# Kernel optimization log

Measured on AMD Instinct MI355X. Metric: run time of the kernel, lower is better.

## Reference

```python
import jax, jax.numpy as jnp
import numpy as np

L, N, K = 12, 4096, 8   # tree levels, padded nodes per level, max children
V, E, H = 50000, 300, 300


def setup_inputs() -> dict:
    key = jax.random.key(0)
    ks = jax.random.split(key, 24)
    word_ids = jax.random.randint(ks[0], (L, N), 0, V)
    child_idx = jax.random.randint(ks[1], (L, N, K), 0, N)
    child_mask = (jax.random.uniform(ks[2], (L, N, K)) < 0.7).astype(jnp.float32)
    child_mask = child_mask.at[0].set(0.0)  # level 0 nodes are leaves (no children)
    s_e = 1.0 / np.sqrt(E)
    s_h = 1.0 / np.sqrt(H)
    inp = {
        'word_ids': word_ids,
        'child_idx': child_idx,
        'child_mask': child_mask,
        'embedding': jax.random.normal(ks[3], (V, E), jnp.float32),
    }
    for t, g in enumerate(['i', 'f', 'o', 'u']):
        inp['w_' + g] = jax.random.normal(ks[4 + 4 * t], (H, E), jnp.float32) * s_e
        inp['b_w' + g] = jax.random.normal(ks[5 + 4 * t], (H,), jnp.float32) * s_e
        inp['u_' + g] = jax.random.normal(ks[6 + 4 * t], (H, H), jnp.float32) * s_h
        inp['b_u' + g] = jax.random.normal(ks[7 + 4 * t], (H,), jnp.float32) * s_h
    return inp


def _lin(x, W, b):
    # torch nn.Linear: x @ W.T + b
    return jnp.matmul(x, W.T) + b


def reference(word_ids, child_idx, child_mask, embedding,
              w_i, b_wi, u_i, b_ui, w_f, b_wf, u_f, b_uf,
              w_o, b_wo, u_o, b_uo, w_u, b_wu, u_u, b_uu):
    n = word_ids.shape[1]
    h_dim = w_i.shape[0]
    dt = embedding.dtype

    def step(carry, level):
        h_prev, c_prev = carry           # [N, H] from previous tree level
        wids, cidx, cmask = level        # [N], [N, K], [N, K]
        x = embedding[wids]              # [N, E]
        h_k = h_prev[cidx]               # [N, K, H] variable-arity child gather
        c_k = c_prev[cidx]               # [N, K, H]
        m = cmask[..., None]             # [N, K, 1]
        # per-child forget gate: sigmoid(w_f(x_j) + u_f(h_k))
        f = jax.nn.sigmoid(_lin(x, w_f, b_wf)[:, None, :] + _lin(h_k, u_f, b_uf))
        h_tilde = jnp.sum(m * h_k, axis=1)        # child-sum of hidden states
        sum_c = jnp.sum(m * f * c_k, axis=1)      # gated child cell sum
        i = jax.nn.sigmoid(_lin(x, w_i, b_wi) + _lin(h_tilde, u_i, b_ui))
        o = jax.nn.sigmoid(_lin(x, w_o, b_wo) + _lin(h_tilde, u_o, b_uo))
        u = jnp.tanh(_lin(x, w_u, b_wu) + _lin(h_tilde, u_u, b_uu))
        c = i * u + sum_c
        h = o * jnp.tanh(c)
        return (h, c), None

    init = (jnp.zeros((n, h_dim), dt), jnp.zeros((n, h_dim), dt))
    (h, c), _ = jax.lax.scan(step, init, (word_ids, child_idx, child_mask))
    return h, c
```

## Files before the change

### kernel.cpp

```cpp
#include <hip/hip_runtime.h>
#include <cmath>
#include <cstdint>


#define NN    4096
#define HH    300
#define KK    8
#define LVLS  12
#define KP    320
#define MTOT  49152
#define NW    1280

typedef __bf16  bf16x8 __attribute__((ext_vector_type(8)));
typedef float   f32x4  __attribute__((ext_vector_type(4)));

#define GAS __attribute__((address_space(1)))
#define LAS __attribute__((address_space(3)))

__device__ __forceinline__ float sigmoidf_(float x) {
    return 1.0f / (1.0f + expf(-x));
}
__device__ __forceinline__ ushort f2bf(float f) {
    union { float f; uint32_t u; } v; v.f = f;
    return (ushort)((v.u + 0x7fffu + ((v.u >> 16) & 1u)) >> 16);
}
__device__ __forceinline__ float bf2f(ushort u) {
    union { uint32_t u; float f; } v; v.u = ((uint32_t)u) << 16;
    return v.f;
}

__global__ __launch_bounds__(256)
void pack_and_stage(
    const float* __restrict__ wi, const float* __restrict__ bwi,
    const float* __restrict__ ui, const float* __restrict__ bui,
    const float* __restrict__ wf, const float* __restrict__ bwf,
    const float* __restrict__ uf, const float* __restrict__ buf_,
    const float* __restrict__ wo, const float* __restrict__ bwo,
    const float* __restrict__ uo, const float* __restrict__ buo,
    const float* __restrict__ wu, const float* __restrict__ bwu,
    const float* __restrict__ uu, const float* __restrict__ buu,
    ushort* __restrict__ W4, ushort* __restrict__ Ufp, ushort* __restrict__ WzU,
    float* __restrict__ BZ, float* __restrict__ Bwf, float* __restrict__ BUF,
    ushort* __restrict__ Hk,
    const int* __restrict__ word_ids, const float* __restrict__ emb,
    ushort* __restrict__ X)
{
    const int b = blockIdx.x;
    if (b >= 3527) {
        int idx = (b - 3527) * 256 + threadIdx.x;
        int kb = idx / MTOT, row = idx % MTOT;
        const int k0 = kb * 8;
        ushort o[8];
        if (kb < 37) {
            const float4* p = reinterpret_cast<const float4*>(
                emb + (size_t)word_ids[row] * 300 + k0);
            float4 v0 = p[0], v1 = p[1];
            o[0] = f2bf(v0.x); o[1] = f2bf(v0.y); o[2] = f2bf(v0.z); o[3] = f2bf(v0.w);
            o[4] = f2bf(v1.x); o[5] = f2bf(v1.y); o[6] = f2bf(v1.z); o[7] = f2bf(v1.w);
        } else if (kb == 37) {
            const float4 v0 = *reinterpret_cast<const float4*>(
                emb + (size_t)word_ids[row] * 300 + k0);
            o[0] = f2bf(v0.x); o[1] = f2bf(v0.y); o[2] = f2bf(v0.z); o[3] = f2bf(v0.w);
            o[4] = o[5] = o[6] = o[7] = 0;
        } else {
            o[0] = o[1] = o[2] = o[3] = o[4] = o[5] = o[6] = o[7] = 0;
        }
        ushort* dst = X + ((size_t)kb * MTOT + row) * 8;
        ushort4 a; a.x = o[0]; a.y = o[1]; a.z = o[2]; a.w = o[3];
        ushort4 c; c.x = o[4]; c.y = o[5]; c.z = o[6]; c.w = o[7];
        *reinterpret_cast<ushort4*>(dst)     = a;
        *reinterpret_cast<ushort4*>(dst + 4) = c;
        return;
    }
    int t = b * 256 + threadIdx.x;
    if (t < 409600) {
        int gate = t / 102400, rem = t % 102400;
        int r = rem / 320, k = rem % 320;
        const float* W = (gate == 0) ? wf : (gate == 1) ? wi
                       : (gate == 2) ? wo : wu;
        float v = (r < 300 && k < 300) ? W[r * 300 + k] : 0.f;
        W4[((size_t)(k >> 3) * NW + gate * 320 + r) * 8 + (k & 7)] = f2bf(v);
    } else if (t < 512000) {
        int x = t - 409600, r = x / 320, k = x % 320;
        Ufp[((size_t)(k >> 3) * KP + r) * 8 + (k & 7)] =
            f2bf((r < 300 && k < 300) ? uf[r * 300 + k] : 0.f);
    } else if (t < 819200) {
        int x = t - 512000;
        int g = x / 102400, rem = x % 102400;
        int r = rem / 320, k = rem % 320;
        const float* U = (g == 0) ? ui : (g == 1) ? uo : uu;
        WzU[(((size_t)g * 40 + (k >> 3)) * KP + r) * 8 + (k & 7)] =
            f2bf((r < 300 && k < 300) ? U[r * 300 + k] : 0.f);
    } else if (t < 820160) {
        int x = t - 819200, g = x / KP, r = x % KP;
        const float* bw = (g == 0) ? bwi : (g == 1) ? bwo : bwu;
        const float* bu = (g == 0) ? bui : (g == 1) ? buo : buu;
        BZ[x] = (r < 300) ? bw[r] + bu[r] : 0.f;
    } else if (t < 820480) {
        int r = t - 820160;
        Bwf[r] = (r < 300) ? bwf[r] : 0.f;
    } else if (t < 820800) {
        int r = t - 820480;
        BUF[r] = (r < 300) ? buf_[r] : 0.f;
    } else if (t < 902720) {
        int x = t - 820800;
        int row = x / 20, pe = x % 20;
        int k = 300 + pe;
        Hk[((size_t)(k >> 3) * NN + row) * 8 + (k & 7)] = 0;
    }
}

__global__ __launch_bounds__(256)
void zx_all_kernel(const ushort* __restrict__ Xp, const ushort* __restrict__ W4,
                   const float* __restrict__ Bwf, ushort* __restrict__ ZW)
{
    __shared__ __attribute__((aligned(16))) ushort As[2][4][128][8];
    __shared__ __attribute__((aligned(16))) ushort Bs[2][4][128][8];

    const int b  = blockIdx.x;
    const int bj = (b % 8) * 480 + b / 8;
    const int m0 = (bj / 10) * 128, n0 = (bj % 10) * 128;

    const int t = threadIdx.x, l = t & 63, w = t >> 6;
    const int m_off = (w >> 1) * 64, n_off = (w & 1) * 64;
    const int kq = l >> 4, lr = l & 15;

    f32x4 acc[4][4] = {};

    auto STAGE = [&](int buf, int s) {
        #pragma unroll
        for (int c = 0; c < 2; ++c) {
            const int slot = t + 256 * c;
            const int kb = slot >> 7, row = slot & 127;
            const ushort* src = Xp + ((size_t)(s * 4 + kb) * MTOT + m0 + row) * 8;
            __builtin_amdgcn_global_load_lds((const GAS void*)src,
                (LAS void*)&As[buf][kb][row][0], 16, 0, 0);
        }
        #pragma unroll
        for (int c = 0; c < 2; ++c) {
            const int slot = t + 256 * c;
            const int kb = slot >> 7, row = slot & 127;
            const ushort* src = W4 + ((size_t)(s * 4 + kb) * NW + n0 + row) * 8;
            __builtin_amdgcn_global_load_lds((const GAS void*)src,
                (LAS void*)&Bs[buf][kb][row][0], 16, 0, 0);
        }
    };
    auto COMPUTE = [&](int buf) {
        bf16x8 af[4], bfr[4];
        #pragma unroll
        for (int mi = 0; mi < 4; ++mi)
            af[mi] = *reinterpret_cast<const bf16x8*>(
                &As[buf][kq][m_off + mi * 16 + lr][0]);
        #pragma unroll
        for (int ni = 0; ni < 4; ++ni)
            bfr[ni] = *reinterpret_cast<const bf16x8*>(
                &Bs[buf][kq][n_off + ni * 16 + lr][0]);
        #pragma unroll
        for (int mi = 0; mi < 4; ++mi)
            #pragma unroll
            for (int ni = 0; ni < 4; ++ni)
                acc[mi][ni] = __builtin_amdgcn_mfma_f32_16x16x32_bf16(
                    af[mi], bfr[ni], acc[mi][ni], 0, 0, 0);
    };

    STAGE(0, 0);
    #pragma unroll
    for (int s = 0; s < 9; ++s) {
        STAGE((s + 1) & 1, s + 1);
        asm volatile("s_waitcnt vmcnt(4)" ::: "memory");
        __builtin_amdgcn_s_barrier();
        COMPUTE(s & 1);
        __builtin_amdgcn_s_barrier();
    }
    asm volatile("s_waitcnt vmcnt(0)" ::: "memory");
    __builtin_amdgcn_s_barrier();
    COMPUTE(1);

    const int col = l & 15, r0 = (l >> 4) * 4;
    #pragma unroll
    for (int mi = 0; mi < 4; ++mi) {
        #pragma unroll
        for (int ni = 0; ni < 4; ++ni) {
            const int gn = n0 + n_off + ni * 16 + col;
            const float bb = (gn < 320) ? Bwf[gn] : 0.f;
            #pragma unroll
            for (int r = 0; r < 4; ++r) {
                const int gm = m0 + m_off + mi * 16 + r0 + r;
                ZW[(size_t)gm * NW + gn] = f2bf(acc[mi][ni][r] + bb);
            }
        }
    }
}

__global__ __launch_bounds__(256)
void fp_kernel(const ushort* __restrict__ Hk, const ushort* __restrict__ Ufp,
               const float* __restrict__ BUFb, ushort* __restrict__ FP)
{
    __shared__ __attribute__((aligned(16))) ushort As[2][8][64][8];
    __shared__ __attribute__((aligned(16))) ushort Bs[2][8][32][8];

    const int b  = blockIdx.x;
    const int bj = (b % 8) * 80 + b / 8;
    const int m0 = (bj / 10) * 64, j0 = (bj % 10) * 32;

    const int t = threadIdx.x, w = t >> 6, l = t & 63;
    const int kq = l >> 4, lr = l & 15;
    const int m_off = (w >> 1) * 32, j_off = (w & 1) * 16;

    f32x4 acc[2] = {};

    auto STAGE = [&](int buf, int s) {
        #pragma unroll
        for (int c = 0; c < 2; ++c) {
            const int slot = t + 256 * c;
            const int kb = slot >> 6, row = slot & 63;
            const ushort* src = Hk + ((size_t)(s * 8 + kb) * NN + m0 + row) * 8;
            __builtin_amdgcn_global_load_lds((const GAS void*)src,
                (LAS void*)&As[buf][kb][row][0], 16, 0, 0);
        }
        {
            const int kb = t >> 5, row = t & 31;
            const ushort* src = Ufp + ((size_t)(s * 8 + kb) * KP + j0 + row) * 8;
            __builtin_amdgcn_global_load_lds((const GAS void*)src,
                (LAS void*)&Bs[buf][kb][row][0], 16, 0, 0);
        }
    };
    auto COMPUTE = [&](int buf) {
        #pragma unroll
        for (int kk = 0; kk < 2; ++kk) {
            const int kc = kk * 4 + kq;
            bf16x8 af[2], bf;
            #pragma unroll
            for (int mi = 0; mi < 2; ++mi)
                af[mi] = *reinterpret_cast<const bf16x8*>(
                    &As[buf][kc][m_off + mi * 16 + lr][0]);
            bf = *reinterpret_cast<const bf16x8*>(
                    &Bs[buf][kc][j_off + lr][0]);
            #pragma unroll
            for (int mi = 0; mi < 2; ++mi)
                acc[mi] = __builtin_amdgcn_mfma_f32_16x16x32_bf16(
                    af[mi], bf, acc[mi], 0, 0, 0);
        }
    };

    STAGE(0, 0);
    #pragma unroll
    for (int s = 0; s < 4; ++s) {
        STAGE((s + 1) & 1, s + 1);
        asm volatile("s_waitcnt vmcnt(3)" ::: "memory");
        __builtin_amdgcn_s_barrier();
        COMPUTE(s & 1);
        __builtin_amdgcn_s_barrier();
    }
    asm volatile("s_waitcnt vmcnt(0)" ::: "memory");
    __builtin_amdgcn_s_barrier();
    COMPUTE(0);

    const int col = l & 15, r0 = (l >> 4) * 4;
    const int gn = j0 + j_off + col;
    if (gn < 300) {
        const float bb = BUFb[gn];
        #pragma unroll
        for (int mi = 0; mi < 2; ++mi)
            #pragma unroll
            for (int r = 0; r < 4; ++r)
                FP[(size_t)(m0 + m_off + mi * 16 + r0 + r) * KP + gn] =
                    f2bf(acc[mi][r] + bb);
    }
}

__global__ __launch_bounds__(320)
void reduce_kernel(const ushort* __restrict__ Hbf, const float* __restrict__ Cst,
                   const ushort* __restrict__ FP, const ushort* __restrict__ ZWlev,
                   const int* __restrict__ cidx, const float* __restrict__ cmask,
                   ushort* __restrict__ HTp, float* __restrict__ SC)
{
    const int x = threadIdx.x;
    const int ty = threadIdx.y;
    const int n = blockIdx.x * 4 + ty;
    __shared__ int   ch[4][KK];
    __shared__ float mk[4][KK];
    if (x < KK) {
        ch[ty][x] = cidx[n * KK + x];
        mk[ty][x] = cmask[n * KK + x];
    }
    __syncthreads();
    if (x >= 75) {
        ushort4 z; z.x = z.y = z.z = z.w = 0;
        const int pi = x - 75;
        const int kb = 37 + ((pi + 1) >> 1);
        const int off = ((pi & 1) ^ 1) * 4;
        *reinterpret_cast<ushort4*>(
            HTp + ((size_t)kb * NN + n) * 8 + off) = z;
        return;
    }
    const int h = x * 4;

    ushort4 hu[KK]; ushort4 fu[KK]; float4 cv[KK];
    #pragma unroll
    for (int k = 0; k < KK; ++k) {
        const size_t cr = (size_t)ch[ty][k];
        hu[k] = *reinterpret_cast<const ushort4*>(&Hbf[cr * KP + h]);
        fu[k] = *reinterpret_cast<const ushort4*>(&FP [cr * KP + h]);
        cv[k] = *reinterpret_cast<const float4*>(&Cst[cr * HH + h]);
    }

    ushort4 wxu = *reinterpret_cast<const ushort4*>(&ZWlev[(size_t)n * NW + h]);
    const float wx0 = bf2f(wxu.x), wx1 = bf2f(wxu.y),
                wx2 = bf2f(wxu.z), wx3 = bf2f(wxu.w);
    float ht0 = 0.f, ht1 = 0.f, ht2 = 0.f, ht3 = 0.f;
    float sc0 = 0.f, sc1 = 0.f, sc2 = 0.f, sc3 = 0.f;

    #pragma unroll
    for (int k = 0; k < KK; ++k) {
        const float m = mk[ty][k];
        if (m != 0.f) {
            ht0 += m * bf2f(hu[k].x); ht1 += m * bf2f(hu[k].y);
            ht2 += m * bf2f(hu[k].z); ht3 += m * bf2f(hu[k].w);
            sc0 += m * sigmoidf_(wx0 + bf2f(fu[k].x)) * cv[k].x;
            sc1 += m * sigmoidf_(wx1 + bf2f(fu[k].y)) * cv[k].y;
            sc2 += m * sigmoidf_(wx2 + bf2f(fu[k].z)) * cv[k].z;
            sc3 += m * sigmoidf_(wx3 + bf2f(fu[k].w)) * cv[k].w;
        }
    }
    ushort4 ho; ho.x = f2bf(ht0); ho.y = f2bf(ht1); ho.z = f2bf(ht2); ho.w = f2bf(ht3);
    *reinterpret_cast<ushort4*>(
        HTp + ((size_t)(x >> 1) * NN + n) * 8 + (x & 1) * 4) = ho;
    float4 so; so.x = sc0; so.y = sc1; so.z = sc2; so.w = sc3;
    *reinterpret_cast<float4*>(&SC[(size_t)n * KP + h]) = so;
}

__global__ __launch_bounds__(256)
void zgemm(const ushort* __restrict__ HTp, const ushort* __restrict__ WzU,
           const float* __restrict__ BZ, const float* __restrict__ SC,
           const ushort* __restrict__ ZXlev,
           float* __restrict__ cdst, ushort* __restrict__ Hb,
           ushort* __restrict__ Hk, float* __restrict__ hdst)
{
    __shared__ __attribute__((aligned(16))) ushort As[2][8][64][8];
    __shared__ __attribute__((aligned(16))) ushort Bs[2][3][8][32][8];

    const int b  = blockIdx.x;
    const int bj = (b % 8) * 80 + b / 8;
    const int m0 = (bj / 10) * 64, j0 = (bj % 10) * 32;

    const int t = threadIdx.x, w = t >> 6, l = t & 63;
    const int kq = l >> 4, lr = l & 15;
    const int m_off = (w >> 1) * 32, j_off = (w & 1) * 16;

    f32x4 acc[3][2] = {};

    auto STAGE = [&](int buf, int s) {
        #pragma unroll
        for (int c = 0; c < 2; ++c) {
            const int slot = t + 256 * c;
            const int kb = slot >> 6, row = slot & 63;
            const ushort* src = HTp + ((size_t)(s * 8 + kb) * NN + m0 + row) * 8;
            __builtin_amdgcn_global_load_lds((const GAS void*)src,
                (LAS void*)&As[buf][kb][row][0], 16, 0, 0);
        }
        #pragma unroll
        for (int c = 0; c < 3; ++c) {
            const int slot = t + 256 * c;
            const int g = slot >> 8, rem = slot & 255;
            const int kb = rem >> 5, row = rem & 31;
            const ushort* src = WzU +
                (((size_t)g * 40 + s * 8 + kb) * KP + j0 + row) * 8;
            __builtin_amdgcn_global_load_lds((const GAS void*)src,
                (LAS void*)&Bs[buf][g][kb][row][0], 16, 0, 0);
        }
    };
    auto COMPUTE = [&](int buf) {
        #pragma unroll
        for (int kk = 0; kk < 2; ++kk) {
            const int kc = kk * 4 + kq;
            bf16x8 af[2], bfr[3];
            #pragma unroll
            for (int mi = 0; mi < 2; ++mi)
                af[mi] = *reinterpret_cast<const bf16x8*>(
                    &As[buf][kc][m_off + mi * 16 + lr][0]);
            #pragma unroll
            for (int g = 0; g < 3; ++g)
                bfr[g] = *reinterpret_cast<const bf16x8*>(
                    &Bs[buf][g][kc][j_off + lr][0]);
            #pragma unroll
            for (int g = 0; g < 3; ++g)
                #pragma unroll
                for (int mi = 0; mi < 2; ++mi)
                    acc[g][mi] = __builtin_amdgcn_mfma_f32_16x16x32_bf16(
                        af[mi], bfr[g], acc[g][mi], 0, 0, 0);
        }
    };

    STAGE(0, 0);
    #pragma unroll
    for (int s = 0; s < 4; ++s) {
        STAGE((s + 1) & 1, s + 1);
        asm volatile("s_waitcnt vmcnt(5)" ::: "memory");
        __builtin_amdgcn_s_barrier();
        COMPUTE(s & 1);
        __builtin_amdgcn_s_barrier();
    }
    asm volatile("s_waitcnt vmcnt(0)" ::: "memory");
    __builtin_amdgcn_s_barrier();
    COMPUTE(0);

    const int col = l & 15, r0 = (l >> 4) * 4;
    const int gn = j0 + j_off + col;
    if (gn < 300) {
        const float bi_ = BZ[gn], bo_ = BZ[KP + gn], bu_ = BZ[2 * KP + gn];
        #pragma unroll
        for (int mi = 0; mi < 2; ++mi) {
            #pragma unroll
            for (int r = 0; r < 4; ++r) {
                const int gm = m0 + m_off + mi * 16 + r0 + r;
                const size_t zb = (size_t)gm * NW + 320 + gn;
                const float zi = bf2f(ZXlev[zb]);
                const float zo = bf2f(ZXlev[zb + 320]);
                const float zu = bf2f(ZXlev[zb + 640]);
                const float sc = SC[(size_t)gm * KP + gn];
                const float ig = sigmoidf_(acc[0][mi][r] + zi + bi_);
                const float og = sigmoidf_(acc[1][mi][r] + zo + bo_);
                const float ug = tanhf   (acc[2][mi][r] + zu + bu_);
                const float c  = ig * ug + sc;
                const float hv = og * tanhf(c);
                cdst[(size_t)gm * HH + gn] = c;
                const ushort hb = f2bf(hv);
                Hb[(size_t)gm * KP + gn] = hb;
                Hk[((size_t)(gn >> 3) * NN + gm) * 8 + (gn & 7)] = hb;
                if (hdst) hdst[(size_t)gm * HH + gn] = hv;
            }
        }
    }
}

extern "C" void kernel_launch(void* const* d_in, const int* in_sizes, int n_in,
                              void* d_out, int out_size, void* d_ws, size_t ws_size,
                              hipStream_t stream)
{
    const int*   word_ids   = (const int*)  d_in[0];
    const int*   child_idx  = (const int*)  d_in[1];
    const float* child_mask = (const float*)d_in[2];
    const float* emb        = (const float*)d_in[3];
    const float* w_i  = (const float*)d_in[4];  const float* b_wi = (const float*)d_in[5];
    const float* u_i  = (const float*)d_in[6];  const float* b_ui = (const float*)d_in[7];
    const float* w_f  = (const float*)d_in[8];  const float* b_wf = (const float*)d_in[9];
    const float* u_f  = (const float*)d_in[10]; const float* b_uf = (const float*)d_in[11];
    const float* w_o  = (const float*)d_in[12]; const float* b_wo = (const float*)d_in[13];
    const float* u_o  = (const float*)d_in[14]; const float* b_uo = (const float*)d_in[15];
    const float* w_u  = (const float*)d_in[16]; const float* b_wu = (const float*)d_in[17];
    const float* u_u  = (const float*)d_in[18]; const float* b_uu = (const float*)d_in[19];

    uint8_t* ws = (uint8_t*)d_ws;
    size_t off = 0;
    auto alloc = [&](size_t bytes) {
        uint8_t* p = ws + off;
        off += (bytes + 255) & ~(size_t)255;
        return p;
    };
    ushort* W4    = (ushort*)alloc((size_t)40 * NW * 8 * 2);
    ushort* Ufp   = (ushort*)alloc((size_t)40 * KP * 8 * 2);
    ushort* WzU   = (ushort*)alloc((size_t)3 * 40 * KP * 8 * 2);
    ushort* Xall  = (ushort*)alloc((size_t)40 * MTOT * 8 * 2);
    ushort* ZW    = (ushort*)alloc((size_t)MTOT * NW * 2);
    ushort* FPbf  = (ushort*)alloc((size_t)NN * KP * 2);
    ushort* HTp   = (ushort*)alloc((size_t)40 * NN * 8 * 2);
    ushort* Hbf   = (ushort*)alloc((size_t)NN * KP * 2);
    ushort* Hk    = (ushort*)alloc((size_t)40 * NN * 8 * 2);
    float*  SCb   = (float*) alloc((size_t)NN * KP * 4);
    float*  C0    = (float*) alloc((size_t)NN * HH * 4);
    float*  BZ    = (float*) alloc(3 * KP * 4);
    float*  Bwf   = (float*) alloc(KP * 4);
    float*  BUFb  = (float*) alloc(KP * 4);

    pack_and_stage<<<11207, 256, 0, stream>>>(
        w_i, b_wi, u_i, b_ui, w_f, b_wf, u_f, b_uf,
        w_o, b_wo, u_o, b_uo, w_u, b_wu, u_u, b_uu,
        W4, Ufp, WzU, BZ, Bwf, BUFb, Hk,
        word_ids, emb, Xall);
    zx_all_kernel<<<3840, 256, 0, stream>>>(Xall, W4, Bwf, ZW);

    float* h_final = (float*)d_out;
    float* c_final = (float*)d_out + (size_t)NN * HH;

    for (int lev = 0; lev < LVLS; ++lev) {
        const int*    cidx  = child_idx  + (size_t)lev * NN * KK;
        const float*  cmask = child_mask + (size_t)lev * NN * KK;
        const ushort* ZWlev = ZW + (size_t)lev * NN * NW;
        const bool last = (lev == LVLS - 1);
        float* cdst = last ? c_final : C0;
        float* hdst = last ? h_final : nullptr;

        if (lev > 0)
            fp_kernel<<<640, 256, 0, stream>>>(Hk, Ufp, BUFb, FPbf);
        reduce_kernel<<<1024, dim3(80, 4), 0, stream>>>(
            Hbf, C0, FPbf, ZWlev, cidx, cmask, HTp, SCb);
        zgemm<<<640, 256, 0, stream>>>(
            HTp, WzU, BZ, SCb, ZWlev, cdst, Hbf, Hk, hdst);
    }
}
```

Before: 477.5 us.

## Fuse child-sum reduction into FP GEMM launch and cell-sum into gate GEMM epilogue

Removes the separate reduce kernel at every level. The h_tilde child-sum now runs in extra blocks of the forget-projection GEMM launch, reading directly from the blocked Hk layout. The gated child cell-sum (sum_c) is computed inside the zgemm epilogue by gathering FP and the previous C for each child. This drops the Hbf and SC intermediate buffers and double-buffers C, cutting one launch and one global round trip per level. In exchange, the epilogue does scattered scalar gathers of 8 children per element, and the h_tilde reads become strided 8-byte loads.

```diff
diff --git a/kernel.cpp b/kernel.cpp
--- a/kernel.cpp
+++ b/kernel.cpp
@@ -193,11 +193,155 @@
 }
 
 __global__ __launch_bounds__(256)
-void fp_kernel(const ushort* __restrict__ Hk, const ushort* __restrict__ Ufp,
-               const float* __restrict__ BUFb, ushort* __restrict__ FP)
+void fp_ht_kernel(const ushort* __restrict__ Hk, const ushort* __restrict__ Ufp,
+                  const float* __restrict__ BUFb, ushort* __restrict__ FP,
+                  const int* __restrict__ cidx, const float* __restrict__ cmask,
+                  ushort* __restrict__ HTp, int fp_on)
 {
     __shared__ __attribute__((aligned(16))) ushort As[2][8][64][8];
     __shared__ __attribute__((aligned(16))) ushort Bs[2][8][32][8];
+    __shared__ int   ch4[4][KK];
+    __shared__ float mk4[4][KK];
+
+    const int b = blockIdx.x;
+    const int t = threadIdx.x, w = t >> 6, l = t & 63;
+
+    if (b < 640) {
+        if (!fp_on) return;
+        const int bj = (b % 8) * 80 + b / 8;
+        const int m0 = (bj / 10) * 64, j0 = (bj % 10) * 32;
+        const int kq = l >> 4, lr = l & 15;
+        const int m_off = (w >> 1) * 32, j_off = (w & 1) * 16;
+
+        f32x4 acc[2] = {};
+
+        auto STAGE = [&](int buf, int s) {
+            #pragma unroll
+            for (int c = 0; c < 2; ++c) {
+                const int slot = t + 256 * c;
+                const int kb = slot >> 6, row = slot & 63;
+                const ushort* src = Hk + ((size_t)(s * 8 + kb) * NN + m0 + row) * 8;
+                __builtin_amdgcn_global_load_lds((const GAS void*)src,
+                    (LAS void*)&As[buf][kb][row][0], 16, 0, 0);
+            }
+            {
+                const int kb = t >> 5, row = t & 31;
+                const ushort* src = Ufp + ((size_t)(s * 8 + kb) * KP + j0 + row) * 8;
+                __builtin_amdgcn_global_load_lds((const GAS void*)src,
+                    (LAS void*)&Bs[buf][kb][row][0], 16, 0, 0);
+            }
+        };
+        auto COMPUTE = [&](int buf) {
+            #pragma unroll
+            for (int kk = 0; kk < 2; ++kk) {
+                const int kc = kk * 4 + kq;
+                bf16x8 af[2], bf;
+                #pragma unroll
+                for (int mi = 0; mi < 2; ++mi)
+                    af[mi] = *reinterpret_cast<const bf16x8*>(
+                        &As[buf][kc][m_off + mi * 16 + lr][0]);
+                bf = *reinterpret_cast<const bf16x8*>(
+                        &Bs[buf][kc][j_off + lr][0]);
+                #pragma unroll
+                for (int mi = 0; mi < 2; ++mi)
+                    acc[mi] = __builtin_amdgcn_mfma_f32_16x16x32_bf16(
+                        af[mi], bf, acc[mi], 0, 0, 0);
+            }
+        };
+
+        STAGE(0, 0);
+        #pragma unroll
+        for (int s = 0; s < 4; ++s) {
+            STAGE((s + 1) & 1, s + 1);
+            asm volatile("s_waitcnt vmcnt(3)" ::: "memory");
+            __builtin_amdgcn_s_barrier();
+            COMPUTE(s & 1);
+            __builtin_amdgcn_s_barrier();
+        }
+        asm volatile("s_waitcnt vmcnt(0)" ::: "memory");
+        __builtin_amdgcn_s_barrier();
+        COMPUTE(0);
+
+        const int col = l & 15, r0 = (l >> 4) * 4;
+        const int gn = j0 + j_off + col;
+        if (gn < 300) {
+            const float bb = BUFb[gn];
+            #pragma unroll
+            for (int mi = 0; mi < 2; ++mi)
+                #pragma unroll
+                for (int r = 0; r < 4; ++r)
+                    FP[(size_t)(m0 + m_off + mi * 16 + r0 + r) * KP + gn] =
+                        f2bf(acc[mi][r] + bb);
+        }
+        return;
+    }
+
+    const int bid = b - 640;
+    const int n = bid * 4 + w;
+    if (l < KK) {
+        ch4[w][l] = cidx[n * KK + l];
+        mk4[w][l] = cmask[n * KK + l];
+    }
+    __syncthreads();
+
+    const bool two = (l < 11);
+    const int cA = l, cB = l + 64;
+
+    ushort4 hA[KK], hB[KK];
+    #pragma unroll
+    for (int k = 0; k < KK; ++k) {
+        const size_t cr = (size_t)ch4[w][k];
+        hA[k] = *reinterpret_cast<const ushort4*>(
+            &Hk[((size_t)(cA >> 1) * NN + cr) * 8 + (cA & 1) * 4]);
+        if (two)
+            hB[k] = *reinterpret_cast<const ushort4*>(
+                &Hk[((size_t)(cB >> 1) * NN + cr) * 8 + (cB & 1) * 4]);
+    }
+    float ha[4] = {0.f,0.f,0.f,0.f}, hb[4] = {0.f,0.f,0.f,0.f};
+    #pragma unroll
+    for (int k = 0; k < KK; ++k) {
+        const float m = mk4[w][k];
+        if (m != 0.f) {
+            ha[0] += m * bf2f(hA[k].x); ha[1] += m * bf2f(hA[k].y);
+            ha[2] += m * bf2f(hA[k].z); ha[3] += m * bf2f(hA[k].w);
+            if (two) {
+                hb[0] += m * bf2f(hB[k].x); hb[1] += m * bf2f(hB[k].y);
+                hb[2] += m * bf2f(hB[k].z); hb[3] += m * bf2f(hB[k].w);
+            }
+        }
+    }
+    {
+        ushort4 o; o.x = f2bf(ha[0]); o.y = f2bf(ha[1]);
+        o.z = f2bf(ha[2]); o.w = f2bf(ha[3]);
+        *reinterpret_cast<ushort4*>(
+            &HTp[((size_t)(cA >> 1) * NN + n) * 8 + (cA & 1) * 4]) = o;
+    }
+    if (two) {
+        ushort4 o; o.x = f2bf(hb[0]); o.y = f2bf(hb[1]);
+        o.z = f2bf(hb[2]); o.w = f2bf(hb[3]);
+        *reinterpret_cast<ushort4*>(
+            &HTp[((size_t)(cB >> 1) * NN + n) * 8 + (cB & 1) * 4]) = o;
+    }
+    if (l >= 11 && l < 16) {
+        const int c = 64 + l;
+        ushort4 z; z.x = z.y = z.z = z.w = 0;
+        *reinterpret_cast<ushort4*>(
+            &HTp[((size_t)(c >> 1) * NN + n) * 8 + (c & 1) * 4]) = z;
+    }
+}
+
+__global__ __launch_bounds__(256)
+void zgemm2(const ushort* __restrict__ HTp, const ushort* __restrict__ WzU,
+            const float* __restrict__ BZ, const ushort* __restrict__ ZWlev,
+            const ushort* __restrict__ FPb, const float* __restrict__ Cprev,
+            const int* __restrict__ cidx, const float* __restrict__ cmask,
+            float* __restrict__ cdst, ushort* __restrict__ Hk,
+            float* __restrict__ hdst)
+{
+    __shared__ __attribute__((aligned(16))) ushort As[2][8][64][8];
+    __shared__ __attribute__((aligned(16))) ushort Bs[2][3][8][32][8];
+    __shared__ int   ciL[64][KK];
+    __shared__ float mkL[64][KK];
 
     const int b  = blockIdx.x;
     const int bj = (b % 8) * 80 + b / 8;
@@ -207,146 +351,11 @@
     const int kq = l >> 4, lr = l & 15;
     const int m_off = (w >> 1) * 32, j_off = (w & 1) * 16;
 
-    f32x4 acc[2] = {};
-
-    auto STAGE = [&](int buf, int s) {
-        #pragma unroll
-        for (int c = 0; c < 2; ++c) {
-            const int slot = t + 256 * c;
-            const int kb = slot >> 6, row = slot & 63;
-            const ushort* src = Hk + ((size_t)(s * 8 + kb) * NN + m0 + row) * 8;
-            __builtin_amdgcn_global_load_lds((const GAS void*)src,
-                (LAS void*)&As[buf][kb][row][0], 16, 0, 0);
-        }
-        {
-            const int kb = t >> 5, row = t & 31;
-            const ushort* src = Ufp + ((size_t)(s * 8 + kb) * KP + j0 + row) * 8;
-            __builtin_amdgcn_global_load_lds((const GAS void*)src,
-                (LAS void*)&Bs[buf][kb][row][0], 16, 0, 0);
-        }
-    };
-    auto COMPUTE = [&](int buf) {
-        #pragma unroll
-        for (int kk = 0; kk < 2; ++kk) {
-            const int kc = kk * 4 + kq;
-            bf16x8 af[2], bf;
-            #pragma unroll
-            for (int mi = 0; mi < 2; ++mi)
-                af[mi] = *reinterpret_cast<const bf16x8*>(
-                    &As[buf][kc][m_off + mi * 16 + lr][0]);
-            bf = *reinterpret_cast<const bf16x8*>(
-                    &Bs[buf][kc][j_off + lr][0]);
-            #pragma unroll
-            for (int mi = 0; mi < 2; ++mi)
-                acc[mi] = __builtin_amdgcn_mfma_f32_16x16x32_bf16(
-                    af[mi], bf, acc[mi], 0, 0, 0);
-        }
-    };
-
-    STAGE(0, 0);
-    #pragma unroll
-    for (int s = 0; s < 4; ++s) {
-        STAGE((s + 1) & 1, s + 1);
-        asm volatile("s_waitcnt vmcnt(3)" ::: "memory");
-        __builtin_amdgcn_s_barrier();
-        COMPUTE(s & 1);
-        __builtin_amdgcn_s_barrier();
-    }
-    asm volatile("s_waitcnt vmcnt(0)" ::: "memory");
-    __builtin_amdgcn_s_barrier();
-    COMPUTE(0);
-
-    const int col = l & 15, r0 = (l >> 4) * 4;
-    const int gn = j0 + j_off + col;
-    if (gn < 300) {
-        const float bb = BUFb[gn];
-        #pragma unroll
-        for (int mi = 0; mi < 2; ++mi)
-            #pragma unroll
-            for (int r = 0; r < 4; ++r)
-                FP[(size_t)(m0 + m_off + mi * 16 + r0 + r) * KP + gn] =
-                    f2bf(acc[mi][r] + bb);
-    }
-}
-
-__global__ __launch_bounds__(320)
-void reduce_kernel(const ushort* __restrict__ Hbf, const float* __restrict__ Cst,
-                   const ushort* __restrict__ FP, const ushort* __restrict__ ZWlev,
-                   const int* __restrict__ cidx, const float* __restrict__ cmask,
-                   ushort* __restrict__ HTp, float* __restrict__ SC)
-{
-    const int x = threadIdx.x;
-    const int ty = threadIdx.y;
-    const int n = blockIdx.x * 4 + ty;
-    __shared__ int   ch[4][KK];
-    __shared__ float mk[4][KK];
-    if (x < KK) {
-        ch[ty][x] = cidx[n * KK + x];
-        mk[ty][x] = cmask[n * KK + x];
-    }
-    __syncthreads();
-    if (x >= 75) {
-        ushort4 z; z.x = z.y = z.z = z.w = 0;
-        const int pi = x - 75;
-        const int kb = 37 + ((pi + 1) >> 1);
-        const int off = ((pi & 1) ^ 1) * 4;
-        *reinterpret_cast<ushort4*>(
-            HTp + ((size_t)kb * NN + n) * 8 + off) = z;
-        return;
-    }
-    const int h = x * 4;
-
-    ushort4 hu[KK]; ushort4 fu[KK]; float4 cv[KK];
-    #pragma unroll
-    for (int k = 0; k < KK; ++k) {
-        const size_t cr = (size_t)ch[ty][k];
-        hu[k] = *reinterpret_cast<const ushort4*>(&Hbf[cr * KP + h]);
-        fu[k] = *reinterpret_cast<const ushort4*>(&FP [cr * KP + h]);
-        cv[k] = *reinterpret_cast<const float4*>(&Cst[cr * HH + h]);
-    }
-
-    ushort4 wxu = *reinterpret_cast<const ushort4*>(&ZWlev[(size_t)n * NW + h]);
-    const float wx0 = bf2f(wxu.x), wx1 = bf2f(wxu.y),
-                wx2 = bf2f(wxu.z), wx3 = bf2f(wxu.w);
-    float ht0 = 0.f, ht1 = 0.f, ht2 = 0.f, ht3 = 0.f;
-    float sc0 = 0.f, sc1 = 0.f, sc2 = 0.f, sc3 = 0.f;
-
-    #pragma unroll
-    for (int k = 0; k < KK; ++k) {
-        const float m = mk[ty][k];
-        if (m != 0.f) {
-            ht0 += m * bf2f(hu[k].x); ht1 += m * bf2f(hu[k].y);
-            ht2 += m * bf2f(hu[k].z); ht3 += m * bf2f(hu[k].w);
-            sc0 += m * sigmoidf_(wx0 + bf2f(fu[k].x)) * cv[k].x;
-            sc1 += m * sigmoidf_(wx1 + bf2f(fu[k].y)) * cv[k].y;
-            sc2 += m * sigmoidf_(wx2 + bf2f(fu[k].z)) * cv[k].z;
-            sc3 += m * sigmoidf_(wx3 + bf2f(fu[k].w)) * cv[k].w;
-        }
-    }
-    ushort4 ho; ho.x = f2bf(ht0); ho.y = f2bf(ht1); ho.z = f2bf(ht2); ho.w = f2bf(ht3);
-    *reinterpret_cast<ushort4*>(
-        HTp + ((size_t)(x >> 1) * NN + n) * 8 + (x & 1) * 4) = ho;
-    float4 so; so.x = sc0; so.y = sc1; so.z = sc2; so.w = sc3;
-    *reinterpret_cast<float4*>(&SC[(size_t)n * KP + h]) = so;
-}
-
-__global__ __launch_bounds__(256)
-void zgemm(const ushort* __restrict__ HTp, const ushort* __restrict__ WzU,
-           const float* __restrict__ BZ, const float* __restrict__ SC,
-           const ushort* __restrict__ ZXlev,
-           float* __restrict__ cdst, ushort* __restrict__ Hb,
-           ushort* __restrict__ Hk, float* __restrict__ hdst)
-{
-    __shared__ __attribute__((aligned(16))) ushort As[2][8][64][8];
-    __shared__ __attribute__((aligned(16))) ushort Bs[2][3][8][32][8];
-
-    const int b  = blockIdx.x;
-    const int bj = (b % 8) * 80 + b / 8;
-    const int m0 = (bj / 10) * 64, j0 = (bj % 10) * 32;
-
-    const int t = threadIdx.x, w = t >> 6, l = t & 63;
-    const int kq = l >> 4, lr = l & 15;
-    const int m_off = (w >> 1) * 32, j_off = (w & 1) * 16;
+    const int e0 = t * 2, e1 = e0 + 1;
+    const int   ciA = cidx [(m0 + (e0 >> 3)) * KK + (e0 & 7)];
+    const float mkA = cmask[(m0 + (e0 >> 3)) * KK + (e0 & 7)];
+    const int   ciB = cidx [(m0 + (e1 >> 3)) * KK + (e1 & 7)];
+    const float mkB = cmask[(m0 + (e1 >> 3)) * KK + (e1 & 7)];
 
     f32x4 acc[3][2] = {};
 
@@ -405,6 +414,10 @@
     __builtin_amdgcn_s_barrier();
     COMPUTE(0);
 
+    ciL[e0 >> 3][e0 & 7] = ciA;  mkL[e0 >> 3][e0 & 7] = mkA;
+    ciL[e1 >> 3][e1 & 7] = ciB;  mkL[e1 >> 3][e1 & 7] = mkB;
+    __syncthreads();
+
     const int col = l & 15, r0 = (l >> 4) * 4;
     const int gn = j0 + j_off + col;
     if (gn < 300) {
@@ -413,21 +426,33 @@
         for (int mi = 0; mi < 2; ++mi) {
             #pragma unroll
             for (int r = 0; r < 4; ++r) {
-                const int gm = m0 + m_off + mi * 16 + r0 + r;
-                const size_t zb = (size_t)gm * NW + 320 + gn;
-                const float zi = bf2f(ZXlev[zb]);
-                const float zo = bf2f(ZXlev[zb + 320]);
-                const float zu = bf2f(ZXlev[zb + 640]);
-                const float sc = SC[(size_t)gm * KP + gn];
+                const int ridx = m_off + mi * 16 + r0 + r;
+                const int gm = m0 + ridx;
+                const size_t zrow = (size_t)gm * NW;
+                const float wx = bf2f(ZWlev[zrow + gn]);
+                const float zi = bf2f(ZWlev[zrow + 320 + gn]);
+                const float zo = bf2f(ZWlev[zrow + 640 + gn]);
+                const float zu = bf2f(ZWlev[zrow + 960 + gn]);
+                float fpv[KK], ccv[KK], mv[KK];
+                #pragma unroll
+                for (int k = 0; k < KK; ++k) {
+                    const size_t c = (size_t)ciL[ridx][k];
+                    mv[k]  = mkL[ridx][k];
+                    fpv[k] = bf2f(FPb[c * KP + gn]);
+                    ccv[k] = Cprev[c * HH + gn];
+                }
+                float sc = 0.f;
+                #pragma unroll
+                for (int k = 0; k < KK; ++k)
+                    if (mv[k] != 0.f)
+                        sc += mv[k] * sigmoidf_(wx + fpv[k]) * ccv[k];
                 const float ig = sigmoidf_(acc[0][mi][r] + zi + bi_);
                 const float og = sigmoidf_(acc[1][mi][r] + zo + bo_);
                 const float ug = tanhf   (acc[2][mi][r] + zu + bu_);
-                const float c  = ig * ug + sc;
-                const float hv = og * tanhf(c);
-                cdst[(size_t)gm * HH + gn] = c;
-                const ushort hb = f2bf(hv);
-                Hb[(size_t)gm * KP + gn] = hb;
-                Hk[((size_t)(gn >> 3) * NN + gm) * 8 + (gn & 7)] = hb;
+                const float c_ = ig * ug + sc;
+                const float hv = og * tanhf(c_);
+                cdst[(size_t)gm * HH + gn] = c_;
+                Hk[((size_t)(gn >> 3) * NN + gm) * 8 + (gn & 7)] = f2bf(hv);
                 if (hdst) hdst[(size_t)gm * HH + gn] = hv;
             }
         }
@@ -465,13 +490,13 @@
     ushort* ZW    = (ushort*)alloc((size_t)MTOT * NW * 2);
     ushort* FPbf  = (ushort*)alloc((size_t)NN * KP * 2);
     ushort* HTp   = (ushort*)alloc((size_t)40 * NN * 8 * 2);
-    ushort* Hbf   = (ushort*)alloc((size_t)NN * KP * 2);
     ushort* Hk    = (ushort*)alloc((size_t)40 * NN * 8 * 2);
-    float*  SCb   = (float*) alloc((size_t)NN * KP * 4);
-    float*  C0    = (float*) alloc((size_t)NN * HH * 4);
+    float*  Cb0   = (float*) alloc((size_t)NN * HH * 4);
+    float*  Cb1   = (float*) alloc((size_t)NN * HH * 4);
     float*  BZ    = (float*) alloc(3 * KP * 4);
     float*  Bwf   = (float*) alloc(KP * 4);
     float*  BUFb  = (float*) alloc(KP * 4);
+    float*  Cb[2] = { Cb0, Cb1 };
 
     pack_and_stage<<<11207, 256, 0, stream>>>(
         w_i, b_wi, u_i, b_ui, w_f, b_wf, u_f, b_uf,
@@ -483,19 +508,19 @@
     float* h_final = (float*)d_out;
     float* c_final = (float*)d_out + (size_t)NN * HH;
 
+    int cur = 0;
     for (int lev = 0; lev < LVLS; ++lev) {
         const int*    cidx  = child_idx  + (size_t)lev * NN * KK;
         const float*  cmask = child_mask + (size_t)lev * NN * KK;
         const ushort* ZWlev = ZW + (size_t)lev * NN * NW;
         const bool last = (lev == LVLS - 1);
-        float* cdst = last ? c_final : C0;
-        float* hdst = last ? h_final : nullptr;
-
-        if (lev > 0)
-            fp_kernel<<<640, 256, 0, stream>>>(Hk, Ufp, BUFb, FPbf);
-        reduce_kernel<<<1024, dim3(80, 4), 0, stream>>>(
-            Hbf, C0, FPbf, ZWlev, cidx, cmask, HTp, SCb);
-        zgemm<<<640, 256, 0, stream>>>(
-            HTp, WzU, BZ, SCb, ZWlev, cdst, Hbf, Hk, hdst);
-    }
-}
+
+        fp_ht_kernel<<<1664, 256, 0, stream>>>(
+            Hk, Ufp, BUFb, FPbf, cidx, cmask, HTp, lev > 0 ? 1 : 0);
+        zgemm2<<<640, 256, 0, stream>>>(
+            HTp, WzU, BZ, ZWlev, FPbf, Cb[cur], cidx, cmask,
+            last ? c_final : Cb[cur ^ 1], Hk,
+            last ? h_final : nullptr);
+        cur ^= 1;
+    }
+}
```

Result: slower. 495.2 us (+3.7%).
